# Optimization experiments

Measured on AMD Instinct MI355X. Metric: run time of the kernel, lower is better.

Reference implementation:

```python
import jax, jax.numpy as jnp
import numpy as np
from functools import partial

K = 1024
EMA_DECAY = 0.99
TOL = 1e-4
EPS = 1e-5
MAX_ITERS = 10


def setup_inputs() -> dict:
    key = jax.random.key(0)
    x = jax.random.normal(key, (32, 256, 1024), dtype=jnp.float32)
    return {"x": x}


def _sq_dists(xf, x_sq, centers):
    # squared euclidean distances [N, K]; argmin is identical to torch.cdist argmin
    c_sq = jnp.sum(centers * centers, axis=1)
    return x_sq[:, None] + c_sq[None, :] - 2.0 * (xf @ centers.T)


def reference(x):
    b, c, t = x.shape
    xf = jnp.transpose(x, (0, 2, 1)).reshape(-1, c)  # [N, c], N = b*t
    N = xf.shape[0]
    # _init_centers: random permutation of rows, take first K (training mode)
    perm = jax.random.permutation(jax.random.key(1), N)[:K]
    ema0 = xf[perm]  # [K, c]
    x_sq = jnp.sum(xf * xf, axis=1)  # [N]
    ones = jnp.ones((N,), dtype=xf.dtype)

    def step(carry, _):
        ema, labels_prev, done = carry
        d = _sq_dists(xf, x_sq, ema)
        labels = jnp.argmin(d, axis=1)  # [N]
        counts = jax.ops.segment_sum(ones, labels, num_segments=K)  # [K]
        sums = jax.ops.segment_sum(xf, labels, num_segments=K)      # [K, c]
        centers = sums / (counts[:, None] + EPS)
        # dead-center handling: keep old ema center where cluster is empty
        centers = jnp.where((counts == 0)[:, None], ema, centers)
        new_ema = ema * EMA_DECAY + (1.0 - EMA_DECAY) * centers
        err = jnp.linalg.norm(new_ema - centers)
        # torch loop breaks AFTER the ema update of the converged iteration;
        # once done, later iterations are no-ops.
        ema_out = jnp.where(done, ema, new_ema)
        labels_out = jnp.where(done, labels_prev, labels)
        new_done = jnp.logical_or(done, err < TOL)
        return (ema_out, labels_out, new_done), None

    init = (ema0, jnp.zeros((N,), dtype=jnp.int32), jnp.array(False))
    (ema, labels, done), _ = jax.lax.scan(step, init, None, length=MAX_ITERS)

    # if loop never broke, torch recomputes labels against final ema centers
    labels_final = jnp.argmin(_sq_dists(xf, x_sq, ema), axis=1)
    return jnp.where(done, labels, labels_final)
```

## Files before the change

### kernel.cpp

```cpp
#include <hip/hip_runtime.h>
#include <stdint.h>

#define JAX_PARTITIONABLE 1

static constexpr int C_ = 256;
static constexpr int T_ = 1024;
static constexpr int N_ = 32768;
static constexpr int K_ = 1024;
static constexpr float MARGIN_ = 0.02f;

typedef __attribute__((ext_vector_type(8))) short short8;
typedef __attribute__((ext_vector_type(4))) float f32x4;

__host__ __device__ __forceinline__ void tf2x32(uint32_t k0, uint32_t k1,
                                                uint32_t x0, uint32_t x1,
                                                uint32_t& o0, uint32_t& o1) {
  const uint32_t ks2 = k0 ^ k1 ^ 0x1BD11BDAu;
  uint32_t v0 = x0 + k0, v1 = x1 + k1;
#define TFR(d) { v0 += v1; v1 = (v1 << d) | (v1 >> (32 - d)); v1 ^= v0; }
#define TF4A TFR(13) TFR(15) TFR(26) TFR(6)
#define TF4B TFR(17) TFR(29) TFR(16) TFR(24)
  TF4A v0 += k1;  v1 += ks2 + 1u;
  TF4B v0 += ks2; v1 += k0 + 2u;
  TF4A v0 += k0;  v1 += k1 + 3u;
  TF4B v0 += k1;  v1 += ks2 + 4u;
  TF4A v0 += ks2; v1 += k0 + 5u;
  o0 = v0; o1 = v1;
#undef TFR
#undef TF4A
#undef TF4B
}

__device__ __forceinline__ uint16_t f2bf(float f) {
  const uint32_t u = __float_as_uint(f);
  return (uint16_t)((u + 0x7FFFu + ((u >> 16) & 1u)) >> 16);
}
__device__ __forceinline__ float bf2f(uint16_t h) {
  return __uint_as_float(((uint32_t)h) << 16);
}

__device__ __forceinline__ void write_bfrag(uint16_t* __restrict__ bH, uint16_t* __restrict__ bL,
                                            int k, int c, float v) {
  const int kt = k >> 4;
  const int lane = (k & 15) + (((c & 31) >> 3) << 4);
  const int ck = c >> 5;
  const int j = c & 7;
  const uint16_t h = f2bf(v);
  const uint16_t l = f2bf(v - bf2f(h));
  const size_t idx = ((((size_t)(kt << 3) + ck) << 6) + lane) * 8 + j;
  bH[idx] = h; bL[idx] = l;
}

__global__ void bits_kernel(uint32_t k0, uint32_t k1, unsigned long long* __restrict__ keys) {
#if JAX_PARTITIONABLE
  const int i = blockIdx.x * 256 + threadIdx.x;
  uint32_t o0, o1; tf2x32(k0, k1, 0u, (uint32_t)i, o0, o1);
  keys[i] = (((unsigned long long)(o0 ^ o1)) << 32) | (unsigned)i;
#else
  const int j = blockIdx.x * 256 + threadIdx.x;
  uint32_t o0, o1; tf2x32(k0, k1, (uint32_t)j, (uint32_t)(j + 16384), o0, o1);
  keys[j]         = (((unsigned long long)o0) << 32) | (unsigned)j;
  keys[j + 16384] = (((unsigned long long)o1) << 32) | (unsigned)(j + 16384);
#endif
}

__global__ void rank_kernel(const unsigned long long* __restrict__ keys, int* __restrict__ rank) {
  const int p = blockIdx.x * 256 + threadIdx.x;
  const unsigned long long my = keys[p];
  const int base = blockIdx.y * 4096;
  int cnt = 0;
  #pragma unroll 8
  for (int j = 0; j < 4096; ++j) cnt += (keys[base + j] < my) ? 1 : 0;
  atomicAdd(&rank[p], cnt);
}

__global__ void scatter1_kernel(const int* __restrict__ rank, int* __restrict__ val) {
  const int p = blockIdx.x * 256 + threadIdx.x;
  val[rank[p]] = p;
}

__global__ void scatter2_kernel(const int* __restrict__ rank, const int* __restrict__ val,
                                int* __restrict__ perm) {
  const int q = blockIdx.x * 256 + threadIdx.x;
  const int r = rank[q];
  if (r < K_) perm[r] = val[q];
}

__global__ void transpose_kernel(const float* __restrict__ x, float* __restrict__ xT) {
  __shared__ float tile[256][33];
  const int tid = threadIdx.x;
  const int b = blockIdx.x >> 5, tt = blockIdx.x & 31;
  const int t0 = tt << 5;
  const float* xb = x + (size_t)b * (C_ * T_) + t0;
  #pragma unroll
  for (int i = 0; i < 32; ++i) {
    const int idx = tid + (i << 8);
    const int c = idx >> 5, p = idx & 31;
    tile[c][p] = xb[(size_t)c * T_ + p];
  }
  __syncthreads();
  float* dst = xT + (((size_t)(b << 10) + t0) << 8);
  #pragma unroll
  for (int p = 0; p < 32; ++p)
    dst[((size_t)p << 8) + tid] = tile[tid][p];
}

__device__ __forceinline__ double block_reduce_256_f64(double v, double* red) {
  #pragma unroll
  for (int s = 1; s < 64; s <<= 1) v += __shfl_xor(v, s, 64);
  if ((threadIdx.x & 63) == 0) red[threadIdx.x >> 6] = v;
  __syncthreads();
  return red[0] + red[1] + red[2] + red[3];
}

__global__ void init_ema_kernel(const float* __restrict__ x, const int* __restrict__ perm,
                                float* __restrict__ ema, uint16_t* __restrict__ bfH,
                                uint16_t* __restrict__ bfL,
                                double* __restrict__ csq, float* __restrict__ csq32) {
  __shared__ double red[4];
  const int k = blockIdx.x, c = threadIdx.x;
  const int n = perm[k];
  const int b = n >> 10, t = n & 1023;
  const float v = x[(size_t)b * (C_ * T_) + (size_t)c * T_ + t];
  ema[((size_t)k << 8) + c] = v;
  write_bfrag(bfH, bfL, k, c, v);
  const double s = block_reduce_256_f64((double)v * (double)v, red);
  if (c == 0) { csq[k] = s; csq32[k] = (float)s; }
}

__global__ void update_kernel(float* __restrict__ ema, uint16_t* __restrict__ bfH,
                              uint16_t* __restrict__ bfL,
                              const double* __restrict__ sums4, const int* __restrict__ counts,
                              double* __restrict__ csq, float* __restrict__ csq32) {
  __shared__ double red[4];
  const int k = blockIdx.x, c = threadIdx.x;
  const size_t idx = ((size_t)k << 8) + c;
  const int cnt = counts[k];
  const float e = ema[idx];
  float center;
  if (cnt == 0) {
    center = e;
  } else {
    double sd = 0.0;
    #pragma unroll
    for (int sl = 0; sl < 4; ++sl) sd += sums4[((size_t)((sl << 10) + k) << 8) + c];
    const float s32 = (float)sd;
    const float denom = __fadd_rn((float)cnt, 1e-5f);
    center = __fdiv_rn(s32, denom);
  }
  const float ne = __fadd_rn(__fmul_rn(e, 0.99f), __fmul_rn(0.01f, center));
  ema[idx] = ne;
  write_bfrag(bfH, bfL, k, c, ne);
  const double s = block_reduce_256_f64((double)ne * (double)ne, red);
  if (c == 0) { csq[k] = s; csq32[k] = (float)s; }
}

__global__ __launch_bounds__(256, 3) void assign_mfma(
    const float* __restrict__ x, const short8* __restrict__ bfH, const short8* __restrict__ bfL,
    const float* __restrict__ csq32, int* __restrict__ labels,
    int* __restrict__ flagidx, int* __restrict__ flagcnt) {
  __shared__ float xstage[128][33];
  __shared__ short8 afrag[2][2][8][64];
  __shared__ float mg_d[4][32], mg_2[4][32];
  __shared__ int   mg_k[4][32];

  const int tid = threadIdx.x;
  const int n0 = blockIdx.x << 5;
  const int b = n0 >> 10, t0 = n0 & 1023;
  const float* xb = x + (size_t)b * (C_ * T_) + t0;

  #pragma unroll
  for (int half = 0; half < 2; ++half) {
    #pragma unroll
    for (int i = 0; i < 16; ++i) {
      const int idx = tid + (i << 8);
      const int c = idx >> 5, p = idx & 31;
      xstage[c][p] = xb[(size_t)((half << 7) + c) * T_ + p];
    }
    __syncthreads();
    #pragma unroll
    for (int i = 0; i < 2; ++i) {
      const int slot = tid + (i << 8);
      const int lane = slot & 63;
      const int ck4 = (slot >> 6) & 3;
      const int mt = slot >> 8;
      const int row = lane & 15;
      const int kof = (lane >> 4) << 3;
      short8 h8, l8;
      #pragma unroll
      for (int j = 0; j < 8; ++j) {
        const float v = xstage[(ck4 << 5) + kof + j][(mt << 4) + row];
        const uint16_t hh = f2bf(v);
        h8[j] = (short)hh;
        l8[j] = (short)f2bf(v - bf2f(hh));
      }
      afrag[0][mt][(half << 2) + ck4][lane] = h8;
      afrag[1][mt][(half << 2) + ck4][lane] = l8;
    }
    __syncthreads();
  }

  const int w = tid >> 6, lane = tid & 63;

  float bd[8], b2[8]; int bk[8];
  #pragma unroll
  for (int s = 0; s < 8; ++s) { bd[s] = 3.0e38f; b2[s] = 3.0e38f; bk[s] = 0; }

  const short8* afH = &afrag[0][0][0][0];
  const short8* afL = &afrag[1][0][0][0];

  #pragma unroll 1
  for (int g = 0; g < 4; ++g) {
    f32x4 acc[2][4];
    #pragma unroll
    for (int m = 0; m < 2; ++m)
      #pragma unroll
      for (int t = 0; t < 4; ++t) acc[m][t] = (f32x4){0.f, 0.f, 0.f, 0.f};

    #pragma unroll 1
    for (int pass = 0; pass < 3; ++pass) {
      const short8* ap = (pass == 2) ? afL : afH;
      const short8* bp = (pass == 1) ? bfL : bfH;
      #pragma unroll 2
      for (int ck = 0; ck < 8; ++ck) {
        const short8 a0 = ap[(ck << 6) + lane];
        const short8 a1 = ap[512 + (ck << 6) + lane];
        const size_t bbase = ((((size_t)(w << 4) + (g << 2)) << 3) + ck) * 64 + lane;
        #pragma unroll
        for (int t = 0; t < 4; ++t) {
          const short8 bf = bp[bbase + (size_t)t * 512];
          acc[0][t] = __builtin_amdgcn_mfma_f32_16x16x32_bf16(a0, bf, acc[0][t], 0, 0, 0);
          acc[1][t] = __builtin_amdgcn_mfma_f32_16x16x32_bf16(a1, bf, acc[1][t], 0, 0, 0);
        }
      }
    }
    #pragma unroll
    for (int t = 0; t < 4; ++t) {
      const int kk = (w << 4) + (g << 2) + t;
      const int k = (kk << 4) + (lane & 15);
      const float cq = csq32[k];
      #pragma unroll
      for (int m = 0; m < 2; ++m)
        #pragma unroll
        for (int r = 0; r < 4; ++r) {
          const float d = cq - 2.0f * acc[m][t][r];
          const int s = (m << 2) + r;
          if (d < bd[s]) { b2[s] = bd[s]; bd[s] = d; bk[s] = k; }
          else if (d < b2[s]) b2[s] = d;
        }
    }
  }

  #pragma unroll
  for (int s = 0; s < 8; ++s) {
    #pragma unroll
    for (int sh = 1; sh < 16; sh <<= 1) {
      const float od = __shfl_xor(bd[s], sh, 64);
      const float o2 = __shfl_xor(b2[s], sh, 64);
      const int   ok = __shfl_xor(bk[s], sh, 64);
      if (od < bd[s] || (od == bd[s] && ok < bk[s])) {
        b2[s] = fminf(o2, bd[s]); bd[s] = od; bk[s] = ok;
      } else {
        b2[s] = fminf(b2[s], od);
      }
    }
  }
  if ((lane & 15) == 0) {
    #pragma unroll
    for (int s = 0; s < 8; ++s) {
      const int m = s >> 2, r = s & 3;
      const int pt = (m << 4) + ((lane >> 4) << 2) + r;
      mg_d[w][pt] = bd[s]; mg_2[w][pt] = b2[s]; mg_k[w][pt] = bk[s];
    }
  }
  __syncthreads();

  if (tid < 32) {
    float fb = mg_d[0][tid], f2 = mg_2[0][tid]; int fk = mg_k[0][tid];
    #pragma unroll
    for (int ww = 1; ww < 4; ++ww) {
      const float od = mg_d[ww][tid], o2 = mg_2[ww][tid]; const int ok = mg_k[ww][tid];
      if (od < fb) { f2 = fminf(fb, o2); fb = od; fk = ok; }
      else f2 = fminf(f2, fminf(od, o2));
    }
    const int n = n0 + tid;
    labels[n] = fk;
    if (f2 - fb <= MARGIN_) { const int p = atomicAdd(flagcnt, 1); flagidx[p] = n; }
  }
}

__global__ void refine_kernel(const float* __restrict__ x, const float* __restrict__ ema,
                              const double* __restrict__ csq,
                              const int* __restrict__ flagidx, const int* __restrict__ flagcnt,
                              int* __restrict__ labels) {
  __shared__ float xr[C_];
  __shared__ double rd[4]; __shared__ int rk[4];
  const int tid = threadIdx.x;
  const int cnt = *flagcnt;
  for (int it = blockIdx.x; it < cnt; it += gridDim.x) {
    const int n = flagidx[it];
    const int b = n >> 10, t = n & 1023;
    xr[tid] = x[(size_t)b * (C_ * T_) + (size_t)tid * T_ + t];
    __syncthreads();
    double bdv = 1e300; int bkv = 0;
    #pragma unroll 1
    for (int r = 0; r < 4; ++r) {
      const int k = (r << 8) + tid;
      const float* er = ema + ((size_t)k << 8);
      double acc = 0.0;
      #pragma unroll 4
      for (int c4 = 0; c4 < 64; ++c4) {
        const float4 ev = *(const float4*)(er + (c4 << 2));
        const float4 xv = *(const float4*)(&xr[c4 << 2]);
        acc = fma((double)xv.x, (double)ev.x, acc);
        acc = fma((double)xv.y, (double)ev.y, acc);
        acc = fma((double)xv.z, (double)ev.z, acc);
        acc = fma((double)xv.w, (double)ev.w, acc);
      }
      const double d = csq[k] - 2.0 * acc;
      if (d < bdv) { bdv = d; bkv = k; }
    }
    #pragma unroll
    for (int s = 1; s < 64; s <<= 1) {
      const double od = __shfl_xor(bdv, s, 64);
      const int    ok = __shfl_xor(bkv, s, 64);
      if (od < bdv || (od == bdv && ok < bkv)) { bdv = od; bkv = ok; }
    }
    if ((tid & 63) == 0) { rd[tid >> 6] = bdv; rk[tid >> 6] = bkv; }
    __syncthreads();
    if (tid == 0) {
      #pragma unroll
      for (int wv = 1; wv < 4; ++wv)
        if (rd[wv] < bdv || (rd[wv] == bdv && rk[wv] < bkv)) { bdv = rd[wv]; bkv = rk[wv]; }
      if (bkv != labels[n]) labels[n] = bkv;
    }
    __syncthreads();
  }
}

__global__ void hist_kernel(const int* __restrict__ labels, int* __restrict__ counts) {
  const int n = blockIdx.x * 256 + threadIdx.x;
  atomicAdd(&counts[labels[n]], 1);
}

__global__ void prefix_kernel(const int* __restrict__ counts, int* __restrict__ offsets,
                              int* __restrict__ cursor) {
  __shared__ int part[256];
  __shared__ int pre[256];
  const int tid = threadIdx.x;
  int v[4]; int s = 0;
  #pragma unroll
  for (int i = 0; i < 4; ++i) { v[i] = counts[(tid << 2) + i]; s += v[i]; }
  part[tid] = s;
  __syncthreads();
  if (tid == 0) { int run = 0; for (int i = 0; i < 256; ++i) { pre[i] = run; run += part[i]; } }
  __syncthreads();
  int run = pre[tid];
  #pragma unroll
  for (int i = 0; i < 4; ++i) {
    offsets[(tid << 2) + i] = run; cursor[(tid << 2) + i] = run; run += v[i];
  }
}

__global__ void scatter_sorted_kernel(const int* __restrict__ labels, int* __restrict__ cursor,
                                      int* __restrict__ sortedIdx) {
  const int n = blockIdx.x * 256 + threadIdx.x;
  const int pos = atomicAdd(&cursor[labels[n]], 1);
  sortedIdx[pos] = n;
}

template<int TRANS>
__global__ void segsum_kernel(const float* __restrict__ x, const float* __restrict__ xT,
                              const int* __restrict__ sortedIdx, const int* __restrict__ offsets,
                              const int* __restrict__ counts, double* __restrict__ sums4) {
  const int k = blockIdx.x >> 2, sl = blockIdx.x & 3;
  const int tid = threadIdx.x;
  const int cnt = counts[k], off = offsets[k];
  const int i0 = (cnt * sl) >> 2, i1 = (cnt * (sl + 1)) >> 2;
  double acc = 0.0;
  int i = i0;
  for (; i + 4 <= i1; i += 4) {
    float v0, v1, v2, v3;
    if (TRANS) {
      const int na = sortedIdx[off + i],     nb = sortedIdx[off + i + 1];
      const int nc = sortedIdx[off + i + 2], nd = sortedIdx[off + i + 3];
      v0 = xT[((size_t)na << 8) + tid]; v1 = xT[((size_t)nb << 8) + tid];
      v2 = xT[((size_t)nc << 8) + tid]; v3 = xT[((size_t)nd << 8) + tid];
    } else {
      const int na = sortedIdx[off + i],     nb = sortedIdx[off + i + 1];
      const int nc = sortedIdx[off + i + 2], nd = sortedIdx[off + i + 3];
      v0 = x[(size_t)(na >> 10) * (C_ * T_) + (size_t)tid * T_ + (na & 1023)];
      v1 = x[(size_t)(nb >> 10) * (C_ * T_) + (size_t)tid * T_ + (nb & 1023)];
      v2 = x[(size_t)(nc >> 10) * (C_ * T_) + (size_t)tid * T_ + (nc & 1023)];
      v3 = x[(size_t)(nd >> 10) * (C_ * T_) + (size_t)tid * T_ + (nd & 1023)];
    }
    acc += (double)v0; acc += (double)v1; acc += (double)v2; acc += (double)v3;
  }
  for (; i < i1; ++i) {
    const int n = sortedIdx[off + i];
    const float v = TRANS ? xT[((size_t)n << 8) + tid]
                          : x[(size_t)(n >> 10) * (C_ * T_) + (size_t)tid * T_ + (n & 1023)];
    acc += (double)v;
  }
  sums4[((size_t)((sl << 10) + k) << 8) + tid] = acc;
}

extern "C" void kernel_launch(void* const* d_in, const int* in_sizes, int n_in,
                              void* d_out, int out_size, void* d_ws, size_t ws_size,
                              hipStream_t stream) {
  const float* x = (const float*)d_in[0];
  int* out = (int*)d_out;
  char* ws = (char*)d_ws;

  float*    ema   = (float*)   (ws + 0);
  uint16_t* bfH   = (uint16_t*)(ws + 1048576);
  uint16_t* bfL   = (uint16_t*)(ws + 1572864);
  double*   sums4 = (double*)  (ws + 2097152);
  unsigned long long* keys = (unsigned long long*)(ws + 2097152);
  int*    rank   = (int*)  (ws + 2359296);
  int*    val1   = (int*)  (ws + 2490368);
  const size_t MISC = 2097152 + 8388608;
  int*    counts  = (int*)  (ws + MISC);
  int*    offsets = (int*)  (ws + MISC + 4096);
  int*    cursor  = (int*)  (ws + MISC + 8192);
  double* csq     = (double*)(ws + MISC + 12288);
  float*  csq32   = (float*) (ws + MISC + 20480);
  int*    perm    = (int*)  (ws + MISC + 24576);
  int*    flagcnt = (int*)  (ws + MISC + 28672);
  int*    flagidx = (int*)  (ws + MISC + 32768);
  int*    sortedIdx = (int*)(ws + MISC + 163840);
  const size_t XT_OFF = 11534336;
  float*  xT      = (float*) (ws + XT_OFF);
  const bool trans_ok = ws_size >= XT_OFF + (size_t)N_ * C_ * 4;

  uint32_t s1h, s1l, s2h, s2l;
  {
#if JAX_PARTITIONABLE
    uint32_t ch, cl;
    tf2x32(0u, 1u, 0u, 0u, ch, cl);
    tf2x32(0u, 1u, 0u, 1u, s1h, s1l);
    tf2x32(ch, cl, 0u, 1u, s2h, s2l);
#else
    uint32_t a0, a1, b0, b1, ch, cl;
    tf2x32(0u, 1u, 0u, 2u, a0, a1); tf2x32(0u, 1u, 1u, 3u, b0, b1);
    ch = a0; cl = b0; s1h = a1; s1l = b1;
    tf2x32(ch, cl, 0u, 2u, a0, a1); tf2x32(ch, cl, 1u, 3u, b0, b1);
    s2h = a1; s2l = b1;
#endif
  }

#if JAX_PARTITIONABLE
  bits_kernel<<<128, 256, 0, stream>>>(s1h, s1l, keys);
#else
  bits_kernel<<<64, 256, 0, stream>>>(s1h, s1l, keys);
#endif
  hipMemsetAsync(rank, 0, N_ * 4, stream);
  rank_kernel<<<dim3(128, 8), 256, 0, stream>>>(keys, rank);
  scatter1_kernel<<<128, 256, 0, stream>>>(rank, val1);

#if JAX_PARTITIONABLE
  bits_kernel<<<128, 256, 0, stream>>>(s2h, s2l, keys);
#else
  bits_kernel<<<64, 256, 0, stream>>>(s2h, s2l, keys);
#endif
  hipMemsetAsync(rank, 0, N_ * 4, stream);
  rank_kernel<<<dim3(128, 8), 256, 0, stream>>>(keys, rank);
  scatter2_kernel<<<128, 256, 0, stream>>>(rank, val1, perm);

  init_ema_kernel<<<K_, 256, 0, stream>>>(x, perm, ema, bfH, bfL, csq, csq32);
  if (trans_ok) transpose_kernel<<<1024, 256, 0, stream>>>(x, xT);

  for (int it = 0; it < 10; ++it) {
    hipMemsetAsync(counts, 0, K_ * 4, stream);
    hipMemsetAsync(flagcnt, 0, 4, stream);
    assign_mfma<<<1024, 256, 0, stream>>>(x, (const short8*)bfH, (const short8*)bfL,
                                          csq32, out, flagidx, flagcnt);
    refine_kernel<<<512, 256, 0, stream>>>(x, ema, csq, flagidx, flagcnt, out);
    hist_kernel<<<128, 256, 0, stream>>>(out, counts);
    prefix_kernel<<<1, 256, 0, stream>>>(counts, offsets, cursor);
    scatter_sorted_kernel<<<128, 256, 0, stream>>>(out, cursor, sortedIdx);
    if (trans_ok)
      segsum_kernel<1><<<4096, 256, 0, stream>>>(x, xT, sortedIdx, offsets, counts, sums4);
    else
      segsum_kernel<0><<<4096, 256, 0, stream>>>(x, xT, sortedIdx, offsets, counts, sums4);
    update_kernel<<<K_, 256, 0, stream>>>(ema, bfH, bfL, sums4, counts, csq, csq32);
  }
  hipMemsetAsync(flagcnt, 0, 4, stream);
  assign_mfma<<<1024, 256, 0, stream>>>(x, (const short8*)bfH, (const short8*)bfL,
                                        csq32, out, flagidx, flagcnt);
  refine_kernel<<<512, 256, 0, stream>>>(x, ema, csq, flagidx, flagcnt, out);
}
```

Measured before the change: 3.112 ms.

## Bucket-sort permutation ranking, widen assign tile to 64 points, warp-scan prefix

Replaces the O(N^2/8) brute-force rank of the random permutation with a 256-bucket histogram, scatter and in-bucket rank, so each key only compares against its own bucket. The assign kernel now handles 64 points per block instead of 32, which doubles reuse of each centroid B-fragment load across four M-tiles. The price is more accumulator registers and larger shared memory, with occupancy hint lowered to 2. The prefix kernel switches to a wave-shuffle scan, and the counts and flagcnt memsets are merged into one contiguous memset.

```diff
diff --git a/kernel.cpp b/kernel.cpp
--- a/kernel.cpp
+++ b/kernel.cpp
@@ -64,26 +64,46 @@
 #endif
 }
 
-__global__ void rank_kernel(const unsigned long long* __restrict__ keys, int* __restrict__ rank) {
-  const int p = blockIdx.x * 256 + threadIdx.x;
-  const unsigned long long my = keys[p];
-  const int base = blockIdx.y * 4096;
+__global__ void bhist_kernel(const unsigned long long* __restrict__ keys, int* __restrict__ bcnt) {
+  const int i = blockIdx.x * 256 + threadIdx.x;
+  atomicAdd(&bcnt[(int)(keys[i] >> 56)], 1);
+}
+
+__global__ void bscan_kernel(const int* __restrict__ bcnt, int* __restrict__ boff,
+                             int* __restrict__ bcur) {
+  if (threadIdx.x == 0) {
+    int run = 0;
+    for (int i = 0; i < 256; ++i) { boff[i] = run; bcur[i] = run; run += bcnt[i]; }
+    boff[256] = run;
+  }
+}
+
+__global__ void bscatter_kernel(const unsigned long long* __restrict__ keys,
+                                int* __restrict__ bcur, unsigned long long* __restrict__ barr) {
+  const int i = blockIdx.x * 256 + threadIdx.x;
+  const unsigned long long k = keys[i];
+  const int pos = atomicAdd(&bcur[(int)(k >> 56)], 1);
+  barr[pos] = k;
+}
+
+template<int ROUND>
+__global__ void brank_kernel(const unsigned long long* __restrict__ barr,
+                             const int* __restrict__ boff,
+                             int* __restrict__ val1, int* __restrict__ perm) {
+  const int i = blockIdx.x * 256 + threadIdx.x;
+  const unsigned long long my = barr[i];
+  const int b = (int)(my >> 56);
+  const int lo = boff[b], hi = boff[b + 1];
   int cnt = 0;
-  #pragma unroll 8
-  for (int j = 0; j < 4096; ++j) cnt += (keys[base + j] < my) ? 1 : 0;
-  atomicAdd(&rank[p], cnt);
-}
-
-__global__ void scatter1_kernel(const int* __restrict__ rank, int* __restrict__ val) {
-  const int p = blockIdx.x * 256 + threadIdx.x;
-  val[rank[p]] = p;
-}
-
-__global__ void scatter2_kernel(const int* __restrict__ rank, const int* __restrict__ val,
-                                int* __restrict__ perm) {
-  const int q = blockIdx.x * 256 + threadIdx.x;
-  const int r = rank[q];
-  if (r < K_) perm[r] = val[q];
+  #pragma unroll 4
+  for (int j = lo; j < hi; ++j) cnt += (barr[j] < my) ? 1 : 0;
+  const int r = lo + cnt;
+  const int idx = (int)(uint32_t)my;
+  if (ROUND == 1) {
+    val1[r] = idx;
+  } else {
+    if (r < K_) perm[r] = val1[idx];
+  }
 }
 
 __global__ void transpose_kernel(const float* __restrict__ x, float* __restrict__ xT) {
@@ -155,67 +175,71 @@
   if (c == 0) { csq[k] = s; csq32[k] = (float)s; }
 }
 
-__global__ __launch_bounds__(256, 3) void assign_mfma(
+#define AF(pl, mt, ck, lane) (((((((pl) << 2) + (mt)) << 3) + (ck)) << 6) + (lane))
+__global__ __launch_bounds__(256, 2) void assign_mfma(
     const float* __restrict__ x, const short8* __restrict__ bfH, const short8* __restrict__ bfL,
     const float* __restrict__ csq32, int* __restrict__ labels,
     int* __restrict__ flagidx, int* __restrict__ flagcnt) {
-  __shared__ float xstage[128][33];
-  __shared__ short8 afrag[2][2][8][64];
-  __shared__ float mg_d[4][32], mg_2[4][32];
-  __shared__ int   mg_k[4][32];
+  __shared__ __align__(16) char smem[81920];
+  short8* afrag = (short8*)smem;
+  float (*xstage)[64] = (float(*)[64])(smem + 65536);
+  float* mg_d = (float*)(smem + 65536);
+  float* mg_2 = mg_d + 256;
+  int*   mg_k = (int*)(mg_2 + 256);
 
   const int tid = threadIdx.x;
-  const int n0 = blockIdx.x << 5;
+  const int n0 = blockIdx.x << 6;
   const int b = n0 >> 10, t0 = n0 & 1023;
   const float* xb = x + (size_t)b * (C_ * T_) + t0;
 
-  #pragma unroll
-  for (int half = 0; half < 2; ++half) {
+  #pragma unroll 1
+  for (int q = 0; q < 4; ++q) {
     #pragma unroll
     for (int i = 0; i < 16; ++i) {
       const int idx = tid + (i << 8);
-      const int c = idx >> 5, p = idx & 31;
-      xstage[c][p] = xb[(size_t)((half << 7) + c) * T_ + p];
+      const int c = idx >> 6, p = idx & 63;
+      xstage[c][p] = xb[(size_t)((q << 6) + c) * T_ + p];
     }
     __syncthreads();
     #pragma unroll
     for (int i = 0; i < 2; ++i) {
       const int slot = tid + (i << 8);
       const int lane = slot & 63;
-      const int ck4 = (slot >> 6) & 3;
-      const int mt = slot >> 8;
+      const int ckh = (slot >> 6) & 1;
+      const int mt = slot >> 7;
       const int row = lane & 15;
       const int kof = (lane >> 4) << 3;
       short8 h8, l8;
       #pragma unroll
       for (int j = 0; j < 8; ++j) {
-        const float v = xstage[(ck4 << 5) + kof + j][(mt << 4) + row];
+        const float v = xstage[(ckh << 5) + kof + j][(mt << 4) + row];
         const uint16_t hh = f2bf(v);
         h8[j] = (short)hh;
         l8[j] = (short)f2bf(v - bf2f(hh));
       }
-      afrag[0][mt][(half << 2) + ck4][lane] = h8;
-      afrag[1][mt][(half << 2) + ck4][lane] = l8;
+      const int ck = (q << 1) + ckh;
+      afrag[AF(0, mt, ck, lane)] = h8;
+      afrag[AF(1, mt, ck, lane)] = l8;
     }
     __syncthreads();
   }
 
   const int w = tid >> 6, lane = tid & 63;
 
-  float bd[8], b2[8]; int bk[8];
-  #pragma unroll
-  for (int s = 0; s < 8; ++s) { bd[s] = 3.0e38f; b2[s] = 3.0e38f; bk[s] = 0; }
-
-  const short8* afH = &afrag[0][0][0][0];
-  const short8* afL = &afrag[1][0][0][0];
+  float bd[16], b2[16]; int bk[16];
+  #pragma unroll
+  for (int s = 0; s < 16; ++s) { bd[s] = 3.0e38f; b2[s] = 3.0e38f; bk[s] = 0; }
+
+  const short8* afH = afrag;
+  const short8* afL = afrag + 2048;
 
   #pragma unroll 1
   for (int g = 0; g < 4; ++g) {
-    f32x4 acc[2][4];
-    #pragma unroll
-    for (int m = 0; m < 2; ++m)
+    f32x4 acc[4][4];
+    #pragma unroll
+    for (int mt = 0; mt < 4; ++mt)
       #pragma unroll
-      for (int t = 0; t < 4; ++t) acc[m][t] = (f32x4){0.f, 0.f, 0.f, 0.f};
+      for (int t = 0; t < 4; ++t) acc[mt][t] = (f32x4){0.f, 0.f, 0.f, 0.f};
 
     #pragma unroll 1
     for (int pass = 0; pass < 3; ++pass) {
@@ -223,28 +247,32 @@
       const short8* bp = (pass == 1) ? bfL : bfH;
       #pragma unroll 2
       for (int ck = 0; ck < 8; ++ck) {
-        const short8 a0 = ap[(ck << 6) + lane];
-        const short8 a1 = ap[512 + (ck << 6) + lane];
+        short8 a0 = ap[(0 << 9) + (ck << 6) + lane];
+        short8 a1 = ap[(1 << 9) + (ck << 6) + lane];
+        short8 a2 = ap[(2 << 9) + (ck << 6) + lane];
+        short8 a3 = ap[(3 << 9) + (ck << 6) + lane];
         const size_t bbase = ((((size_t)(w << 4) + (g << 2)) << 3) + ck) * 64 + lane;
         #pragma unroll
         for (int t = 0; t < 4; ++t) {
           const short8 bf = bp[bbase + (size_t)t * 512];
           acc[0][t] = __builtin_amdgcn_mfma_f32_16x16x32_bf16(a0, bf, acc[0][t], 0, 0, 0);
           acc[1][t] = __builtin_amdgcn_mfma_f32_16x16x32_bf16(a1, bf, acc[1][t], 0, 0, 0);
+          acc[2][t] = __builtin_amdgcn_mfma_f32_16x16x32_bf16(a2, bf, acc[2][t], 0, 0, 0);
+          acc[3][t] = __builtin_amdgcn_mfma_f32_16x16x32_bf16(a3, bf, acc[3][t], 0, 0, 0);
         }
       }
     }
     #pragma unroll
     for (int t = 0; t < 4; ++t) {
-      const int kk = (w << 4) + (g << 2) + t;
-      const int k = (kk << 4) + (lane & 15);
+      const int kt = (w << 4) + (g << 2) + t;
+      const int k = (kt << 4) + (lane & 15);
       const float cq = csq32[k];
       #pragma unroll
-      for (int m = 0; m < 2; ++m)
+      for (int mt = 0; mt < 4; ++mt)
         #pragma unroll
         for (int r = 0; r < 4; ++r) {
-          const float d = cq - 2.0f * acc[m][t][r];
-          const int s = (m << 2) + r;
+          const float d = cq - 2.0f * acc[mt][t][r];
+          const int s = (mt << 2) + r;
           if (d < bd[s]) { b2[s] = bd[s]; bd[s] = d; bk[s] = k; }
           else if (d < b2[s]) b2[s] = d;
         }
@@ -252,7 +280,7 @@
   }
 
   #pragma unroll
-  for (int s = 0; s < 8; ++s) {
+  for (int s = 0; s < 16; ++s) {
     #pragma unroll
     for (int sh = 1; sh < 16; sh <<= 1) {
       const float od = __shfl_xor(bd[s], sh, 64);
@@ -267,19 +295,20 @@
   }
   if ((lane & 15) == 0) {
     #pragma unroll
-    for (int s = 0; s < 8; ++s) {
-      const int m = s >> 2, r = s & 3;
-      const int pt = (m << 4) + ((lane >> 4) << 2) + r;
-      mg_d[w][pt] = bd[s]; mg_2[w][pt] = b2[s]; mg_k[w][pt] = bk[s];
+    for (int s = 0; s < 16; ++s) {
+      const int mt = s >> 2, r = s & 3;
+      const int pt = (mt << 4) + ((lane >> 4) << 2) + r;
+      mg_d[(w << 6) + pt] = bd[s]; mg_2[(w << 6) + pt] = b2[s]; mg_k[(w << 6) + pt] = bk[s];
     }
   }
   __syncthreads();
 
-  if (tid < 32) {
-    float fb = mg_d[0][tid], f2 = mg_2[0][tid]; int fk = mg_k[0][tid];
+  if (tid < 64) {
+    float fb = mg_d[tid], f2 = mg_2[tid]; int fk = mg_k[tid];
     #pragma unroll
     for (int ww = 1; ww < 4; ++ww) {
-      const float od = mg_d[ww][tid], o2 = mg_2[ww][tid]; const int ok = mg_k[ww][tid];
+      const float od = mg_d[(ww << 6) + tid], o2 = mg_2[(ww << 6) + tid];
+      const int ok = mg_k[(ww << 6) + tid];
       if (od < fb) { f2 = fminf(fb, o2); fb = od; fk = ok; }
       else f2 = fminf(f2, fminf(od, o2));
     }
@@ -345,21 +374,28 @@
 
 __global__ void prefix_kernel(const int* __restrict__ counts, int* __restrict__ offsets,
                               int* __restrict__ cursor) {
-  __shared__ int part[256];
-  __shared__ int pre[256];
+  __shared__ int wsum[4];
   const int tid = threadIdx.x;
-  int v[4]; int s = 0;
-  #pragma unroll
-  for (int i = 0; i < 4; ++i) { v[i] = counts[(tid << 2) + i]; s += v[i]; }
-  part[tid] = s;
+  const int lane = tid & 63, w = tid >> 6;
+  const int c0 = counts[(tid << 2)], c1 = counts[(tid << 2) + 1];
+  const int c2 = counts[(tid << 2) + 2], c3 = counts[(tid << 2) + 3];
+  const int s = c0 + c1 + c2 + c3;
+  int inc = s;
+  #pragma unroll
+  for (int sh = 1; sh < 64; sh <<= 1) {
+    const int t = __shfl_up(inc, sh, 64);
+    if (lane >= sh) inc += t;
+  }
+  if (lane == 63) wsum[w] = inc;
   __syncthreads();
-  if (tid == 0) { int run = 0; for (int i = 0; i < 256; ++i) { pre[i] = run; run += part[i]; } }
-  __syncthreads();
-  int run = pre[tid];
-  #pragma unroll
-  for (int i = 0; i < 4; ++i) {
-    offsets[(tid << 2) + i] = run; cursor[(tid << 2) + i] = run; run += v[i];
-  }
+  int wof = 0;
+  #pragma unroll
+  for (int i = 0; i < 4; ++i) if (i < w) wof += wsum[i];
+  int run = wof + inc - s;
+  offsets[(tid << 2)] = run;     cursor[(tid << 2)] = run;     run += c0;
+  offsets[(tid << 2) + 1] = run; cursor[(tid << 2) + 1] = run; run += c1;
+  offsets[(tid << 2) + 2] = run; cursor[(tid << 2) + 2] = run; run += c2;
+  offsets[(tid << 2) + 3] = run; cursor[(tid << 2) + 3] = run;
 }
 
 __global__ void scatter_sorted_kernel(const int* __restrict__ labels, int* __restrict__ cursor,
@@ -417,18 +453,21 @@
   uint16_t* bfL   = (uint16_t*)(ws + 1572864);
   double*   sums4 = (double*)  (ws + 2097152);
   unsigned long long* keys = (unsigned long long*)(ws + 2097152);
-  int*    rank   = (int*)  (ws + 2359296);
-  int*    val1   = (int*)  (ws + 2490368);
+  unsigned long long* barr = (unsigned long long*)(ws + 2097152 + 262144);
+  int*    val1   = (int*)  (ws + 2097152 + 524288);
   const size_t MISC = 2097152 + 8388608;
   int*    counts  = (int*)  (ws + MISC);
-  int*    offsets = (int*)  (ws + MISC + 4096);
-  int*    cursor  = (int*)  (ws + MISC + 8192);
-  double* csq     = (double*)(ws + MISC + 12288);
-  float*  csq32   = (float*) (ws + MISC + 20480);
-  int*    perm    = (int*)  (ws + MISC + 24576);
-  int*    flagcnt = (int*)  (ws + MISC + 28672);
+  int*    flagcnt = (int*)  (ws + MISC + 4096);
+  int*    offsets = (int*)  (ws + MISC + 8192);
+  int*    cursor  = (int*)  (ws + MISC + 12288);
+  double* csq     = (double*)(ws + MISC + 16384);
+  float*  csq32   = (float*) (ws + MISC + 24576);
+  int*    perm    = (int*)  (ws + MISC + 28672);
   int*    flagidx = (int*)  (ws + MISC + 32768);
   int*    sortedIdx = (int*)(ws + MISC + 163840);
+  int*    bcnt    = (int*)  (ws + MISC + 294912);
+  int*    boff    = (int*)  (ws + MISC + 295936);
+  int*    bcur    = (int*)  (ws + MISC + 297984);
   const size_t XT_OFF = 11534336;
   float*  xT      = (float*) (ws + XT_OFF);
   const bool trans_ok = ws_size >= XT_OFF + (size_t)N_ * C_ * 4;
@@ -454,27 +493,30 @@
 #else
   bits_kernel<<<64, 256, 0, stream>>>(s1h, s1l, keys);
 #endif
-  hipMemsetAsync(rank, 0, N_ * 4, stream);
-  rank_kernel<<<dim3(128, 8), 256, 0, stream>>>(keys, rank);
-  scatter1_kernel<<<128, 256, 0, stream>>>(rank, val1);
+  hipMemsetAsync(bcnt, 0, 1024, stream);
+  bhist_kernel<<<128, 256, 0, stream>>>(keys, bcnt);
+  bscan_kernel<<<1, 64, 0, stream>>>(bcnt, boff, bcur);
+  bscatter_kernel<<<128, 256, 0, stream>>>(keys, bcur, barr);
+  brank_kernel<1><<<128, 256, 0, stream>>>(barr, boff, val1, perm);
 
 #if JAX_PARTITIONABLE
   bits_kernel<<<128, 256, 0, stream>>>(s2h, s2l, keys);
 #else
   bits_kernel<<<64, 256, 0, stream>>>(s2h, s2l, keys);
 #endif
-  hipMemsetAsync(rank, 0, N_ * 4, stream);
-  rank_kernel<<<dim3(128, 8), 256, 0, stream>>>(keys, rank);
-  scatter2_kernel<<<128, 256, 0, stream>>>(rank, val1, perm);
+  hipMemsetAsync(bcnt, 0, 1024, stream);
+  bhist_kernel<<<128, 256, 0, stream>>>(keys, bcnt);
+  bscan_kernel<<<1, 64, 0, stream>>>(bcnt, boff, bcur);
+  bscatter_kernel<<<128, 256, 0, stream>>>(keys, bcur, barr);
+  brank_kernel<2><<<128, 256, 0, stream>>>(barr, boff, val1, perm);
 
   init_ema_kernel<<<K_, 256, 0, stream>>>(x, perm, ema, bfH, bfL, csq, csq32);
   if (trans_ok) transpose_kernel<<<1024, 256, 0, stream>>>(x, xT);
 
   for (int it = 0; it < 10; ++it) {
-    hipMemsetAsync(counts, 0, K_ * 4, stream);
-    hipMemsetAsync(flagcnt, 0, 4, stream);
-    assign_mfma<<<1024, 256, 0, stream>>>(x, (const short8*)bfH, (const short8*)bfL,
-                                          csq32, out, flagidx, flagcnt);
+    hipMemsetAsync(counts, 0, 8192, stream);
+    assign_mfma<<<512, 256, 0, stream>>>(x, (const short8*)bfH, (const short8*)bfL,
+                                         csq32, out, flagidx, flagcnt);
     refine_kernel<<<512, 256, 0, stream>>>(x, ema, csq, flagidx, flagcnt, out);
     hist_kernel<<<128, 256, 0, stream>>>(out, counts);
     prefix_kernel<<<1, 256, 0, stream>>>(counts, offsets, cursor);
@@ -486,7 +528,7 @@
     update_kernel<<<K_, 256, 0, stream>>>(ema, bfH, bfL, sums4, counts, csq, csq32);
   }
   hipMemsetAsync(flagcnt, 0, 4, stream);
-  assign_mfma<<<1024, 256, 0, stream>>>(x, (const short8*)bfH, (const short8*)bfL,
-                                        csq32, out, flagidx, flagcnt);
+  assign_mfma<<<512, 256, 0, stream>>>(x, (const short8*)bfH, (const short8*)bfL,
+                                       csq32, out, flagidx, flagcnt);
   refine_kernel<<<512, 256, 0, stream>>>(x, ema, csq, flagidx, flagcnt, out);
 }
```

Result: no change. 3.073 ms (-1.3%).
